# Performance work log

Measured on AMD Instinct MI355X. Metric: run time of the kernel, lower is better.

The kernel has to match this reference:

```python
import math
import jax, jax.numpy as jnp
import numpy as np

N = 10000      # num_nodes
E = 320000     # num_edges (avg degree 32)
D = 256        # hidden_dim
H = 8          # num_heads
HD = D // H    # head_dim = 32
S = 3          # num_scales
SCALES = (1.0, 2.0, 4.0)
BASE_MD = 500.0   # max_distance
RADIUS = 50.0     # spatial density radius


def setup_inputs() -> dict:
    key = jax.random.key(0)
    ks = jax.random.split(key, 24)
    nrm = lambda k, shape, s=0.02: jax.random.normal(k, shape, jnp.float32) * s
    return {
        "x": jax.random.normal(ks[0], (N, D), jnp.float32),
        "coords": jax.random.uniform(ks[1], (N, 2), jnp.float32) * 1000.0,
        "edge_index": jax.random.randint(ks[2], (2, E), 0, N, jnp.int32),
        "Wq": nrm(ks[3], (S, D, D)),
        "Wk": nrm(ks[4], (S, D, D)),
        "Wv": nrm(ks[5], (S, D, D)),
        "Wo": nrm(ks[6], (S, D, D)),
        "bo": jnp.zeros((S, D), jnp.float32),
        "temp": jnp.ones((S, H), jnp.float32),
        "dist_emb": nrm(ks[7], (S, 100, HD // 2)),
        "dir_emb": nrm(ks[8], (S, 16, HD // 2)),
        "Wsp1": nrm(ks[9], (S, HD, HD)),
        "bsp1": jnp.zeros((S, HD), jnp.float32),
        "Wsp2": nrm(ks[10], (S, 1, HD)),
        "bsp2": jnp.zeros((S, 1), jnp.float32),
        "Wd1": nrm(ks[11], (S, D // 2, 3)),
        "bd1": jnp.zeros((S, D // 2), jnp.float32),
        "Wd2": nrm(ks[12], (S, D, D // 2)),
        "bd2": jnp.zeros((S, D), jnp.float32),
        "Wf": nrm(ks[13], (D, S * D)),
        "bf": jnp.zeros((D,), jnp.float32),
    }


def reference(x, coords, edge_index, Wq, Wk, Wv, Wo, bo, temp, dist_emb, dir_emb,
              Wsp1, bsp1, Wsp2, bsp2, Wd1, bd1, Wd2, bd2, Wf, bf):
    src, dst = edge_index[0], edge_index[1]   # row=source j, col/dst=target i
    n = x.shape[0]
    eps = 1e-8

    # ---- shared density statistics (same math in every scale's encoder) ----
    ones_e = jnp.ones(src.shape[0], jnp.float32)
    deg = jax.ops.segment_sum(ones_e, src, num_segments=n)
    deg_n = deg / (deg.max() + eps)
    # spatial density: count of neighbors within RADIUS via full cdist (as in torch)
    c = jax.lax.stop_gradient(coords)  # only used via thresholds / integer bins -> zero grad
    d2 = jnp.sqrt(jnp.maximum(((c[:, None, :] - c[None, :, :]) ** 2).sum(-1), 0.0))
    sp = (d2 <= RADIUS).sum(axis=1).astype(jnp.float32) - 1.0
    sp = sp / (sp.max() + eps)
    # local feature variance
    nbr_sum = jax.ops.segment_sum(x[dst], src, num_segments=n)
    cnt = jnp.maximum(deg, 1.0)[:, None]
    fvar = jnp.linalg.norm(x - nbr_sum / cnt, axis=-1)
    fvar = fvar / (fvar.max() + eps)
    dens_raw = jnp.stack([deg_n, sp, fvar], axis=-1)  # [N, 3]

    # ---- shared relative geometry (binned -> no grad through coords) ----
    rel = c[src] - c[dst]                       # coords_j - coords_i
    dist = jnp.linalg.norm(rel, axis=-1)        # [E]
    ang = jnp.arctan2(rel[:, 1], rel[:, 0])
    abin = jnp.clip(((ang + math.pi) / (2.0 * math.pi) * 15.0).astype(jnp.int32), 0, 15)

    outs = []
    for s in range(S):
        md = BASE_MD * SCALES[s]
        dbin = jnp.clip((dist / md * 99.0).astype(jnp.int32), 0, 99)
        se = jnp.concatenate([dist_emb[s][dbin], dir_emb[s][abin]], axis=-1)  # [E, HD]
        enc = (jax.nn.relu(se @ Wsp1[s].T + bsp1[s]) @ Wsp2[s].T + bsp2[s])[:, 0]  # [E]

        df = jax.nn.relu(dens_raw @ Wd1[s].T + bd1[s]) @ Wd2[s].T + bd2[s]  # [N, D]

        q = (x @ Wq[s].T).reshape(n, H, HD)
        k = (x @ Wk[s].T).reshape(n, H, HD)
        v = (x @ Wv[s].T).reshape(n, H, HD)

        scores = (q[dst] * k[src]).sum(-1) / math.sqrt(HD)  # [E, H]
        scores = scores / temp[s][None, :]
        scores = scores + enc[:, None]
        dfi, dfj = df[dst], df[src]
        dsim = (dfi * dfj).sum(-1) / (jnp.maximum(jnp.linalg.norm(dfi, axis=-1), eps)
                                       * jnp.maximum(jnp.linalg.norm(dfj, axis=-1), eps))
        scores = scores * (1.0 + 0.5 * dsim[:, None])

        # scatter-softmax over edges grouped by destination node
        smax = jax.ops.segment_max(scores, dst, num_segments=n)
        p = jnp.exp(scores - smax[dst])
        z = jax.ops.segment_sum(p, dst, num_segments=n)
        probs = p / (z[dst] + 1e-16)

        agg = jax.ops.segment_sum(probs[..., None] * v[src], dst, num_segments=n)
        outs.append(agg.reshape(n, D) @ Wo[s].T + bo[s])

    fused = jnp.concatenate(outs, axis=-1) @ Wf.T + bf
    return fused
```

## Files before the change

kernel.cpp:

```cpp
#include <hip/hip_runtime.h>

typedef _Float16 f16;
typedef _Float16 f16x4 __attribute__((ext_vector_type(4)));
typedef _Float16 f16x8 __attribute__((ext_vector_type(8)));
typedef float    f32x4 __attribute__((ext_vector_type(4)));
typedef float    fv2   __attribute__((ext_vector_type(2)));

__device__ __forceinline__ float4 ld4h(const f16* p) {
  f16x4 t = *(const f16x4*)p;
  return make_float4((float)t[0], (float)t[1], (float)t[2], (float)t[3]);
}

__device__ __forceinline__ float4 dec_fp8x4(unsigned u) {
  fv2 lo = __builtin_amdgcn_cvt_pk_f32_fp8(u, false);
  fv2 hi = __builtin_amdgcn_cvt_pk_f32_fp8(u, true);
  return make_float4(lo[0], lo[1], hi[0], hi[1]);
}

__device__ __forceinline__ unsigned enc_fp8x4(float a, float b, float c, float d) {
  unsigned v = 0;
  v = __builtin_amdgcn_cvt_pk_fp8_f32(a, b, v, false);
  v = __builtin_amdgcn_cvt_pk_fp8_f32(c, d, v, true);
  return v;
}

__device__ __forceinline__ void gld_lds16(const void* g, void* l) {
  __builtin_amdgcn_global_load_lds(
      (const __attribute__((address_space(1))) unsigned*)g,
      (__attribute__((address_space(3))) unsigned*)l, 16, 0, 0);
}

__device__ __forceinline__ int cell_of(const float* coords, int i) {
  int cx = (int)(coords[2 * i] * 0.02f);
  int cy = (int)(coords[2 * i + 1] * 0.02f);
  cx = cx < 0 ? 0 : (cx > 19 ? 19 : cx);
  cy = cy < 0 ? 0 : (cy > 19 ? 19 : cy);
  return cy * 20 + cx;
}

__global__ __launch_bounds__(256) void prep_kernel(
    const float* __restrict__ x, const float* __restrict__ Wq, const float* __restrict__ Wk,
    const float* __restrict__ Wv, const float* __restrict__ Wd2,
    f16* __restrict__ x_h, unsigned* __restrict__ x8, f16* __restrict__ wqvk,
    f16* __restrict__ wd2h,
    const float* __restrict__ dist_emb, const float* __restrict__ dir_emb,
    const float* __restrict__ Wsp1, const float* __restrict__ bsp1,
    const float* __restrict__ Wsp2, const float* __restrict__ bsp2,
    float* __restrict__ enc_tab,
    const int* __restrict__ eidx, const float* __restrict__ coords,
    int* deg_i, int* indeg_i, int* cellcnt, int E, int N)
{
  const int b = blockIdx.x;
  if (b < 2048) {
    const int n0 = N * 64;
    const int total = n0 + 147456 + 24576;
    for (int i = b * 256 + threadIdx.x; i < total; i += 2048 * 256) {
      int k = i;
      if (k < n0) {
        float4 v = ((const float4*)x)[k];
        f16x4 o; o[0] = (f16)v.x; o[1] = (f16)v.y; o[2] = (f16)v.z; o[3] = (f16)v.w;
        ((f16x4*)x_h)[k] = o;
        x8[k] = enc_fp8x4(v.x, v.y, v.z, v.w);
        continue;
      }
      const float4* sp; f16x4* dp;
      k -= n0;
      if (k < 147456) {
        int s = k / 49152, r = k % 49152, m = r / 16384, off = r % 16384;
        const float* w = (m == 0) ? Wq : (m == 1) ? Wk : Wv;
        int dblk = (m == 0) ? 0 : (m == 1) ? 32768 : 16384;
        sp = (const float4*)(w + s * 65536) + off;
        dp = (f16x4*)wqvk + s * 49152 + dblk + off;
      } else {
        k -= 147456;
        sp = (const float4*)Wd2 + k; dp = (f16x4*)wd2h + k;
      }
      float4 v = *sp;
      f16x4 o; o[0] = (f16)v.x; o[1] = (f16)v.y; o[2] = (f16)v.z; o[3] = (f16)v.w;
      *dp = o;
    }
  } else if (b < 2067) {
    int id = (b - 2048) * 256 + threadIdx.x;
    if (id >= 3 * 1600) return;
    int s = id / 1600, c = id % 1600, db = c >> 4, ab = c & 15;
    const float* de = dist_emb + (size_t)(s * 100 + db) * 16;
    const float* ae = dir_emb + (size_t)(s * 16 + ab) * 16;
    const float* w1 = Wsp1 + s * 1024;
    const float* b1 = bsp1 + s * 32;
    const float* w2 = Wsp2 + s * 32;
    float enc = bsp2[s];
    for (int j = 0; j < 32; ++j) {
      float a = b1[j];
      const float* wr = w1 + j * 32;
#pragma unroll
      for (int i = 0; i < 16; ++i) a += de[i] * wr[i];
#pragma unroll
      for (int i = 0; i < 16; ++i) a += ae[i] * wr[16 + i];
      enc += fmaxf(a, 0.0f) * w2[j];
    }
    enc_tab[id] = enc;
  } else {
    int e = (b - 2067) * 256 + threadIdx.x;
    if (e < E) {
      atomicAdd(&deg_i[eidx[e]], 1);
      atomicAdd(&indeg_i[eidx[E + e]], 1);
    }
    if (e < N) atomicAdd(&cellcnt[cell_of(coords, e)], 1);
  }
}

__global__ __launch_bounds__(256) void wfo_kernel(
    const float* __restrict__ Wf, const float* __restrict__ Wo,
    const float* __restrict__ bo, const float* __restrict__ bf,
    f16* __restrict__ wfo, float* __restrict__ bias_f)
{
  const int j = threadIdx.x;
  if (blockIdx.y == 3) {
    if (blockIdx.x != 0) return;
    float acc = bf[j];
    const float* wr = Wf + (size_t)j * 768;
    for (int t = 0; t < 768; ++t) acc = fmaf(bo[t], wr[t], acc);
    bias_f[j] = acc;
    return;
  }
  __shared__ float wrow[256];
  const int o = blockIdx.x, s = blockIdx.y;
  wrow[j] = Wf[o * 768 + s * 256 + j];
  __syncthreads();
  const float* wo = Wo + (size_t)s * 65536 + j;
  float acc = 0.f;
#pragma unroll 8
  for (int m = 0; m < 256; ++m) acc = fmaf(wrow[m], wo[(size_t)m * 256], acc);
  wfo[(size_t)o * 768 + s * 256 + j] = (f16)acc;
}

__global__ __launch_bounds__(1024) void scan_kernel(const int* __restrict__ indeg,
                                                    const int* __restrict__ deg,
                                                    const int* __restrict__ cellcnt,
                                                    int* dptr, int* sptr, int* cptr,
                                                    int* __restrict__ perm, int N)
{
  __shared__ int lds[1024];
  __shared__ int cnt[256], scn2[256], fill[256];
  const int tid = threadIdx.x;
  const int pass = blockIdx.x;
  if (pass == 3) {
    if (tid < 256) { cnt[tid] = 0; fill[tid] = 0; }
    __syncthreads();
    for (int n = tid; n < N; n += 1024) {
      int d = indeg[n];
      int key = 255 - (d > 255 ? 255 : d);
      atomicAdd(&cnt[key], 1);
    }
    __syncthreads();
    if (tid < 256) scn2[tid] = cnt[tid];
    __syncthreads();
    for (int off = 1; off < 256; off <<= 1) {
      int v = 0;
      if (tid < 256 && tid >= off) v = scn2[tid - off];
      __syncthreads();
      if (tid < 256) scn2[tid] += v;
      __syncthreads();
    }
    for (int n = tid; n < N; n += 1024) {
      int d = indeg[n];
      int key = 255 - (d > 255 ? 255 : d);
      int pos = scn2[key] - cnt[key] + atomicAdd(&fill[key], 1);
      perm[pos] = n;
    }
    return;
  }
  const int* in = (pass == 0) ? indeg : (pass == 1) ? deg : cellcnt;
  int* out = (pass == 0) ? dptr : (pass == 1) ? sptr : cptr;
  int len = (pass == 2) ? 400 : N;
  int base = tid * 16;
  int loc[16];
  int sum = 0;
#pragma unroll
  for (int j = 0; j < 16; ++j) {
    int v = (base + j < len) ? in[base + j] : 0;
    loc[j] = sum; sum += v;
  }
  lds[tid] = sum;
  __syncthreads();
  for (int off = 1; off < 1024; off <<= 1) {
    int t = (tid >= off) ? lds[tid - off] : 0;
    __syncthreads();
    lds[tid] += t;
    __syncthreads();
  }
  int prev = tid ? lds[tid - 1] : 0;
#pragma unroll
  for (int j = 0; j < 16; ++j)
    if (base + j < len) out[base + j] = prev + loc[j];
  if (tid == 1023) out[len] = lds[1023];
}

__global__ __launch_bounds__(256) void scatter_kernel(
    const int* __restrict__ eidx, const float* __restrict__ coords,
    const int* __restrict__ dptr, const int* __restrict__ sptr, const int* __restrict__ cptr,
    int* fill_d, int* fill_s, int* fill_c,
    int2* __restrict__ erec, int* __restrict__ sdst, float2* __restrict__ scoord, int E, int N)
{
  int e = blockIdx.x * 256 + threadIdx.x;
  if (e < E) {
    int s = eidx[e], d = eidx[E + e];
    float rx = coords[2 * s] - coords[2 * d];
    float ry = coords[2 * s + 1] - coords[2 * d + 1];
    float dist = sqrtf(rx * rx + ry * ry);
    float ang = atan2f(ry, rx);
    int ab = (int)((ang + 3.14159265358979323846f) / 6.28318530717958647692f * 15.0f);
    ab = ab < 0 ? 0 : (ab > 15 ? 15 : ab);
    int b0 = (int)((dist / 500.0f) * 99.0f);  b0 = b0 < 0 ? 0 : (b0 > 99 ? 99 : b0);
    int b1 = (int)((dist / 1000.0f) * 99.0f); b1 = b1 < 0 ? 0 : (b1 > 99 ? 99 : b1);
    int b2 = (int)((dist / 2000.0f) * 99.0f); b2 = b2 < 0 ? 0 : (b2 > 99 ? 99 : b2);
    unsigned pb = (unsigned)b0 | ((unsigned)b1 << 7) | ((unsigned)b2 << 14) | ((unsigned)ab << 21);
    int pd = dptr[d] + atomicAdd(&fill_d[d], 1);
    erec[pd] = make_int2(s, (int)pb);
    int ps = sptr[s] + atomicAdd(&fill_s[s], 1);
    sdst[ps] = d;
  }
  if (e < N) {
    int cid = cell_of(coords, e);
    int pc = cptr[cid] + atomicAdd(&fill_c[cid], 1);
    scoord[pc] = ((const float2*)coords)[e];
  }
}

__global__ __launch_bounds__(256) void node_stats_kernel(
    const float* __restrict__ coords, const float2* __restrict__ scoord,
    const int* __restrict__ cptr,
    const float* __restrict__ x, const unsigned* __restrict__ x8,
    const int* __restrict__ sptr, const int* __restrict__ sdst,
    int* __restrict__ sp_i, float* __restrict__ fvar, int N)
{
  int wv = threadIdx.x >> 6, lane = threadIdx.x & 63;
  int node = blockIdx.x * 4 + wv;
  if (node >= N) return;

  float cx = coords[2 * node], cy = coords[2 * node + 1];
  {
    int gx = (int)(cx * 0.02f); gx = gx < 0 ? 0 : (gx > 19 ? 19 : gx);
    int gy = (int)(cy * 0.02f); gy = gy < 0 ? 0 : (gy > 19 ? 19 : gy);
    int x0 = gx > 0 ? gx - 1 : 0, x1 = gx < 19 ? gx + 1 : 19;
    int y0 = gy > 0 ? gy - 1 : 0, y1 = gy < 19 ? gy + 1 : 19;
    int cnt = 0;
    for (int r = y0; r <= y1; ++r) {
      int j0 = cptr[r * 20 + x0], j1 = cptr[r * 20 + x1 + 1];
      for (int j = j0 + lane; j < j1; j += 64) {
        float2 c = scoord[j];
        float dx = cx - c.x, dy = cy - c.y;
        cnt += (dx * dx + dy * dy <= 2500.0f) ? 1 : 0;
      }
    }
    cnt += __shfl_xor(cnt, 1);  cnt += __shfl_xor(cnt, 2);  cnt += __shfl_xor(cnt, 4);
    cnt += __shfl_xor(cnt, 8);  cnt += __shfl_xor(cnt, 16); cnt += __shfl_xor(cnt, 32);
    if (lane == 0) sp_i[node] = cnt;
  }

  const int slot = lane >> 3, w = lane & 7;
  float sum[32];
#pragma unroll
  for (int i = 0; i < 32; ++i) sum[i] = 0.f;
  int e0 = sptr[node], e1 = sptr[node + 1];
  int nit = (e1 - e0 + 7) >> 3;
  for (int it = 0; it < nit; ++it) {
    int e = e0 + it * 8 + slot;
    bool valid = e < e1;
    int dd = sdst[valid ? e : e1 - 1];
    const unsigned* xp = x8 + dd * 64 + w * 8;
    uint4 a = *(const uint4*)xp;
    uint4 b = *(const uint4*)(xp + 4);
    float vm = valid ? 1.f : 0.f;
    unsigned wd[8] = {a.x, a.y, a.z, a.w, b.x, b.y, b.z, b.w};
#pragma unroll
    for (int k = 0; k < 8; ++k) {
      float4 f = dec_fp8x4(wd[k]);
      sum[k*4+0] = fmaf(vm, f.x, sum[k*4+0]);
      sum[k*4+1] = fmaf(vm, f.y, sum[k*4+1]);
      sum[k*4+2] = fmaf(vm, f.z, sum[k*4+2]);
      sum[k*4+3] = fmaf(vm, f.w, sum[k*4+3]);
    }
  }
#pragma unroll
  for (int i = 0; i < 32; ++i) {
    sum[i] += __shfl_xor(sum[i], 8);
    sum[i] += __shfl_xor(sum[i], 16);
    sum[i] += __shfl_xor(sum[i], 32);
  }
  float rcnt = 1.0f / fmaxf((float)(e1 - e0), 1.0f);
  const float4* xp4 = (const float4*)(x + (size_t)node * 256 + w * 32);
  float ss = 0.f;
#pragma unroll
  for (int k = 0; k < 8; ++k) {
    float4 xm = xp4[k];
    float d0 = xm.x - sum[k*4+0] * rcnt;
    float d1 = xm.y - sum[k*4+1] * rcnt;
    float d2 = xm.z - sum[k*4+2] * rcnt;
    float d3 = xm.w - sum[k*4+3] * rcnt;
    ss += d0*d0 + d1*d1 + d2*d2 + d3*d3;
  }
  ss += __shfl_xor(ss, 1);  ss += __shfl_xor(ss, 2);  ss += __shfl_xor(ss, 4);
  ss += __shfl_xor(ss, 8);  ss += __shfl_xor(ss, 16); ss += __shfl_xor(ss, 32);
  if (lane == 0) fvar[node] = sqrtf(ss * 0.125f);
}

__global__ __launch_bounds__(1024) void maxred_kernel(
    const int* __restrict__ sptr, const int* __restrict__ sp_i,
    const float* __restrict__ fvar, float* __restrict__ maxf, int N)
{
  __shared__ float l0[1024], l1[1024], l2[1024];
  int tid = threadIdx.x;
  float m0 = 0.f, m1 = 0.f, m2 = 0.f;
  for (int i = tid; i < N; i += 1024) {
    m0 = fmaxf(m0, (float)(sptr[i + 1] - sptr[i]));
    m1 = fmaxf(m1, (float)(sp_i[i] - 1));
    m2 = fmaxf(m2, fvar[i]);
  }
  l0[tid] = m0; l1[tid] = m1; l2[tid] = m2;
  __syncthreads();
  for (int off = 512; off > 0; off >>= 1) {
    if (tid < off) {
      l0[tid] = fmaxf(l0[tid], l0[tid + off]);
      l1[tid] = fmaxf(l1[tid], l1[tid + off]);
      l2[tid] = fmaxf(l2[tid], l2[tid + off]);
    }
    __syncthreads();
  }
  if (tid == 0) { maxf[0] = l0[0]; maxf[1] = l1[0]; maxf[2] = l2[0]; }
}

__global__ __launch_bounds__(256) void h_kernel(
    const int* __restrict__ sptr, const int* __restrict__ sp_i, const float* __restrict__ fvar,
    const float* __restrict__ maxf, const float* __restrict__ Wd1,
    const float* __restrict__ bd1, f16* __restrict__ hbuf, int N, int Mp)
{
  int id = blockIdx.x * 256 + threadIdx.x;
  if (id >= N * 128) return;
  int s = blockIdx.y;
  int node = id >> 7, j = id & 127;
  float dm = maxf[0] + 1e-8f;
  float sm = maxf[1] + 1e-8f;
  float fm = maxf[2] + 1e-8f;
  float d0 = (float)(sptr[node + 1] - sptr[node]) / dm;
  float d1 = (float)(sp_i[node] - 1) / sm;
  float d2 = fvar[node] / fm;
  const float* wr = Wd1 + s * 384 + j * 3;
  float h = fmaxf(wr[0] * d0 + wr[1] * d1 + wr[2] * d2 + bd1[s * 128 + j], 0.0f);
  hbuf[(size_t)s * Mp * 128 + (size_t)node * 128 + j] = (f16)h;
}

__global__ __launch_bounds__(256) void gemm_bt_f16(
    const f16* __restrict__ A, int lda, long sA,
    const f16* __restrict__ B, int ldb, long sB,
    const float* __restrict__ bias, int sBias,
    void* __restrict__ Cv, int ldc, long sC, int K, int Mstore, int outMode,
    unsigned char* __restrict__ Cv2, int ldc2, long sC2, int ysplit)
{
  __shared__ f16 As[128 * 64];
  __shared__ f16 Bs[128 * 64];
  const int s = blockIdx.z;
  const int tid = threadIdx.x;
  const int lane = tid & 63;
  const int w = tid >> 6;
  const int wr = (w >> 1) * 64, wc = (w & 1) * 64;
  const int srow = tid >> 3;
  const int scol = (((tid & 7) ^ (srow & 7))) * 8;
  const f16* Ab = A + (size_t)s * sA + (size_t)(blockIdx.x * 128 + srow) * lda + scol;
  const f16* Bb = B + (size_t)s * sB + (size_t)(blockIdx.y * 128 + srow) * ldb + scol;
  char* Asl = (char*)As + tid * 16;
  char* Bsl = (char*)Bs + tid * 16;

  f32x4 acc[4][4] = {};

  for (int kt = 0; kt < K; kt += 64) {
    __syncthreads();
#pragma unroll
    for (int i = 0; i < 4; ++i) {
      gld_lds16(Ab + (size_t)i * 32 * lda + kt, Asl + i * 4096);
      gld_lds16(Bb + (size_t)i * 32 * ldb + kt, Bsl + i * 4096);
    }
    __syncthreads();
#pragma unroll
    for (int kq = 0; kq < 2; ++kq) {
      const int krd = kq * 32 + (lane >> 4) * 8;
      const int kc = krd >> 3;
      f16x8 af[4], bfr[4];
#pragma unroll
      for (int t = 0; t < 4; ++t) {
        const int ra = wr + t * 16 + (lane & 15);
        const int rb = wc + t * 16 + (lane & 15);
        af[t]  = *(const f16x8*)&As[ra * 64 + (kc ^ (ra & 7)) * 8];
        bfr[t] = *(const f16x8*)&Bs[rb * 64 + (kc ^ (rb & 7)) * 8];
      }
#pragma unroll
      for (int mi = 0; mi < 4; ++mi)
#pragma unroll
        for (int ni = 0; ni < 4; ++ni)
          acc[mi][ni] = __builtin_amdgcn_mfma_f32_16x16x32_f16(af[mi], bfr[ni], acc[mi][ni], 0, 0, 0);
    }
  }

  const int r0 = (lane >> 4) << 2;
  const int c0 = lane & 15;
  const bool f8p = ((int)blockIdx.y >= ysplit);
  const int cbase = f8p ? ((int)blockIdx.y - ysplit) * 128 : (int)blockIdx.y * 128;
#pragma unroll
  for (int mi = 0; mi < 4; ++mi) {
#pragma unroll
    for (int ni = 0; ni < 4; ++ni) {
      int col = cbase + wc + ni * 16 + c0;
      float bv = (!f8p && bias) ? bias[s * sBias + col] : 0.0f;
#pragma unroll
      for (int r = 0; r < 4; ++r) {
        int row = blockIdx.x * 128 + wr + mi * 16 + r0 + r;
        if (row < Mstore) {
          float v = acc[mi][ni][r] + bv;
          if (f8p) {
            unsigned pk = __builtin_amdgcn_cvt_pk_fp8_f32(v, v, 0u, false);
            Cv2[(size_t)s * sC2 + (size_t)row * ldc2 + col] = (unsigned char)(pk & 0xffu);
          } else if (outMode == 1) {
            ((f16*)Cv)[(size_t)s * sC + (size_t)row * ldc + col] = (f16)v;
          } else {
            ((float*)Cv)[(size_t)s * sC + (size_t)row * ldc + col] = v;
          }
        }
      }
    }
  }
}

__global__ __launch_bounds__(256) void norm_kernel(const f16* __restrict__ dfh,
                                                   unsigned* __restrict__ drec8, int N, int Mp)
{
  int wv = threadIdx.x >> 6, lane = threadIdx.x & 63;
  int node = blockIdx.x * 4 + wv;
  if (node >= N) return;
  int s = blockIdx.y;
  float4 d = ld4h(dfh + (size_t)s * Mp * 256 + (size_t)node * 256 + lane * 4);
  float ss = d.x * d.x + d.y * d.y + d.z * d.z + d.w * d.w;
  ss += __shfl_xor(ss, 1);  ss += __shfl_xor(ss, 2);  ss += __shfl_xor(ss, 4);
  ss += __shfl_xor(ss, 8);  ss += __shfl_xor(ss, 16); ss += __shfl_xor(ss, 32);
  float rn = 1.0f / fmaxf(sqrtf(ss), 1e-8f);
  drec8[(size_t)s * Mp * 64 + node * 64 + lane] = enc_fp8x4(d.x * rn, d.y * rn, d.z * rn, d.w * rn);
}

__global__ __launch_bounds__(256) void edge_attn(
    const f16* __restrict__ nrec0, const unsigned* __restrict__ krec0,
    const unsigned* __restrict__ drec0, const int2* __restrict__ erec,
    const int* __restrict__ dptr, const int* __restrict__ perm,
    const float* __restrict__ enc_tab, const float* __restrict__ temp,
    f16* __restrict__ aggc, int N, int Mp)
{
  int wv = threadIdx.x >> 6, lane = threadIdx.x & 63;
  int node = blockIdx.x * 4 + wv;
  if (node >= N) return;
  node = perm[node];
  const int s = blockIdx.y;
  const int sshift = 7 * s;
  const f16* nrec = nrec0 + (size_t)s * Mp * 512;
  const unsigned* krec8 = krec0 + (size_t)s * Mp * 64;
  const unsigned* drec8 = drec0 + (size_t)s * Mp * 64;
  const float* enc_s = enc_tab + s * 1600;

  const int slot = lane >> 4;
  const int sub  = lane & 15;
  const int hd   = sub >> 1;
  const int half = sub & 1;
  const int doff = hd * 8 + half * 4;
  const int voff = hd * 32 + half * 16;

  float qf[16];
  {
    const f16* qp = nrec + (size_t)node * 512 + voff;
    f16x8 a = *(const f16x8*)qp;
    f16x8 b = *(const f16x8*)(qp + 8);
#pragma unroll
    for (int j = 0; j < 8; ++j) { qf[j] = (float)a[j]; qf[8 + j] = (float)b[j]; }
  }
  uint4 diw = *(const uint4*)(drec8 + node * 64 + doff);
  const float inv_th = 0.17677669529663687f / temp[s * 8 + hd];

  float m = -1e30f, z = 0.f;
  float acc[16];
#pragma unroll
  for (int i = 0; i < 16; ++i) acc[i] = 0.f;

  int e0 = dptr[node], e1 = dptr[node + 1];
  int nit = (e1 - e0 + 3) >> 2;
  for (int it = 0; it < nit; ++it) {
    int e = e0 + it * 4 + slot;
    bool valid = e < e1;
    int2 rec = erec[valid ? e : e1 - 1];
    int src = rec.x;
    unsigned pb = (unsigned)rec.y;
    uint4 kwv = *(const uint4*)(krec8 + src * 64 + doff);
    uint4 dwv = *(const uint4*)(drec8 + src * 64 + doff);
    const f16* vp = nrec + (size_t)src * 512 + 256 + voff;
    f16x8 vs0 = *(const f16x8*)vp;
    f16x8 vs1 = *(const f16x8*)(vp + 8);
    float enc = enc_s[((pb >> sshift) & 127u) * 16 + (pb >> 21)];

    unsigned kw[4] = {kwv.x, kwv.y, kwv.z, kwv.w};
    unsigned dw[4] = {dwv.x, dwv.y, dwv.z, dwv.w};
    unsigned di[4] = {diw.x, diw.y, diw.z, diw.w};
    float qk0 = 0.f, qk1 = 0.f, ds0 = 0.f, ds1 = 0.f;
#pragma unroll
    for (int w = 0; w < 4; ++w) {
      float4 kf = dec_fp8x4(kw[w]);
      qk0 = fmaf(qf[w*4+0], kf.x, qk0);
      qk1 = fmaf(qf[w*4+1], kf.y, qk1);
      qk0 = fmaf(qf[w*4+2], kf.z, qk0);
      qk1 = fmaf(qf[w*4+3], kf.w, qk1);
      float4 df = dec_fp8x4(dw[w]);
      float4 dd = dec_fp8x4(di[w]);
      ds0 = fmaf(dd.x, df.x, ds0);
      ds1 = fmaf(dd.y, df.y, ds1);
      ds0 = fmaf(dd.z, df.z, ds0);
      ds1 = fmaf(dd.w, df.w, ds1);
    }
    float qk = qk0 + qk1;
    float ds = ds0 + ds1;
    qk += __shfl_xor(qk, 1);
    ds += __shfl_xor(ds, 1); ds += __shfl_xor(ds, 2);
    ds += __shfl_xor(ds, 4); ds += __shfl_xor(ds, 8);

    float sc = (qk * inv_th + enc) * (1.0f + 0.5f * ds);
    sc = valid ? sc : -1e30f;
    if (__any(sc > m + 8.0f)) {
      float mn = fmaxf(m, sc);
      float rs = __expf(m - mn);
      z *= rs;
#pragma unroll
      for (int i = 0; i < 16; ++i) acc[i] *= rs;
      m = mn;
    }
    float p = __expf(sc - m) * (valid ? 1.0f : 0.0f);
    z += p;
#pragma unroll
    for (int j = 0; j < 8; ++j) acc[j]     = fmaf(p, (float)vs0[j], acc[j]);
#pragma unroll
    for (int j = 0; j < 8; ++j) acc[8 + j] = fmaf(p, (float)vs1[j], acc[8 + j]);
  }

  float M = m;
  M = fmaxf(M, __shfl_xor(M, 16));
  M = fmaxf(M, __shfl_xor(M, 32));
  float f = __expf(m - M);
  z *= f;
  z += __shfl_xor(z, 16); z += __shfl_xor(z, 32);
#pragma unroll
  for (int i = 0; i < 16; ++i) {
    float a = acc[i] * f;
    a += __shfl_xor(a, 16); a += __shfl_xor(a, 32);
    acc[i] = a;
  }
  float rz = 1.0f / (z + 1e-16f);
  if (slot == 0) {
    f16* op = aggc + (size_t)node * 768 + s * 256 + voff;
    f16x8 o0, o1;
#pragma unroll
    for (int j = 0; j < 8; ++j) { o0[j] = (f16)(acc[j] * rz); o1[j] = (f16)(acc[8 + j] * rz); }
    *(f16x8*)op = o0;
    *(f16x8*)(op + 8) = o1;
  }
}

extern "C" void kernel_launch(void* const* d_in, const int* in_sizes, int n_in,
                              void* d_out, int out_size, void* d_ws, size_t ws_size,
                              hipStream_t stream)
{
  const float* x      = (const float*)d_in[0];
  const float* coords = (const float*)d_in[1];
  const int*   eidx   = (const int*)  d_in[2];
  const float* Wq   = (const float*)d_in[3];
  const float* Wk   = (const float*)d_in[4];
  const float* Wv   = (const float*)d_in[5];
  const float* Wo   = (const float*)d_in[6];
  const float* bo   = (const float*)d_in[7];
  const float* temp = (const float*)d_in[8];
  const float* dist_emb = (const float*)d_in[9];
  const float* dir_emb  = (const float*)d_in[10];
  const float* Wsp1 = (const float*)d_in[11];
  const float* bsp1 = (const float*)d_in[12];
  const float* Wsp2 = (const float*)d_in[13];
  const float* bsp2 = (const float*)d_in[14];
  const float* Wd1  = (const float*)d_in[15];
  const float* bd1  = (const float*)d_in[16];
  const float* Wd2  = (const float*)d_in[17];
  const float* bd2  = (const float*)d_in[18];
  const float* Wf   = (const float*)d_in[19];
  const float* bf   = (const float*)d_in[20];
  (void)n_in; (void)out_size; (void)ws_size;

  const int N  = in_sizes[0] / 256;
  const int E  = in_sizes[2] / 2;
  const int Mp = ((N + 127) / 128) * 128;

  char* p = (char*)d_ws;
  auto alloc = [&](size_t b) -> void* {
    void* r = (void*)p;
    p += (b + 255) & ~(size_t)255;
    return r;
  };

  f16*      x_h   = (f16*)     alloc((size_t)Mp * 256 * 2);
  unsigned* x8    = (unsigned*)alloc((size_t)Mp * 256);
  f16*      nrec3 = (f16*)     alloc((size_t)3 * Mp * 512 * 2);
  unsigned* krec3 = (unsigned*)alloc((size_t)3 * Mp * 256);
  unsigned* drec3 = (unsigned*)alloc((size_t)3 * Mp * 256);
  f16*      hbuf3 = (f16*)     alloc((size_t)3 * Mp * 128 * 2);
  f16*      dfh3  = (f16*)     alloc((size_t)3 * Mp * 256 * 2);
  f16*      aggc  = (f16*)     alloc((size_t)Mp * 768 * 2);
  f16*      wqvk  = (f16*)     alloc((size_t)3 * 768 * 256 * 2);
  f16*      wfo   = (f16*)     alloc((size_t)256 * 768 * 2);
  float*    bias_f = (float*)  alloc(256 * 4);
  f16*      wd2h  = (f16*)     alloc((size_t)3 * 256 * 128 * 2);
  float*    enc_tab = (float*) alloc((size_t)3 * 1600 * 4);
  int*    dptr = (int*)   alloc((size_t)(N + 1) * 4);
  int*    sptr = (int*)   alloc((size_t)(N + 1) * 4);
  int*    cptr = (int*)   alloc((size_t)401 * 4);
  int*    perm = (int*)   alloc((size_t)N * 4);
  int2*   erec = (int2*)  alloc((size_t)E * 8);
  int*    sdst = (int*)   alloc((size_t)E * 4);
  float2* scoord = (float2*)alloc((size_t)N * 8);
  float*  fvar = (float*) alloc((size_t)N * 4);
  int*    sp_i = (int*)   alloc((size_t)N * 4);
  float*  maxf = (float*) alloc(4 * 4);
  char* z0 = p;
  int* deg_i   = (int*)alloc((size_t)N * 4);
  int* indeg_i = (int*)alloc((size_t)N * 4);
  int* fill_d  = (int*)alloc((size_t)N * 4);
  int* fill_s  = (int*)alloc((size_t)N * 4);
  int* cellcnt = (int*)alloc(400 * 4);
  int* fill_c  = (int*)alloc(400 * 4);
  size_t zbytes = (size_t)(p - z0);
  hipMemsetAsync(z0, 0, zbytes, stream);

  {
    int histBlocks = (E + 255) / 256;
    prep_kernel<<<2067 + histBlocks, 256, 0, stream>>>(
        x, Wq, Wk, Wv, Wd2, x_h, x8, wqvk, wd2h,
        dist_emb, dir_emb, Wsp1, bsp1, Wsp2, bsp2, enc_tab,
        eidx, coords, deg_i, indeg_i, cellcnt, E, N);
  }
  wfo_kernel<<<dim3(256, 4), 256, 0, stream>>>(Wf, Wo, bo, bf, wfo, bias_f);
  scan_kernel<<<4, 1024, 0, stream>>>(indeg_i, deg_i, cellcnt, dptr, sptr, cptr, perm, N);
  scatter_kernel<<<(E + 255) / 256, 256, 0, stream>>>(eidx, coords, dptr, sptr, cptr,
                                                      fill_d, fill_s, fill_c, erec, sdst, scoord, E, N);
  node_stats_kernel<<<(N + 3) / 4, 256, 0, stream>>>(coords, scoord, cptr, x, x8,
                                                     sptr, sdst, sp_i, fvar, N);
  maxred_kernel<<<1, 1024, 0, stream>>>(sptr, sp_i, fvar, maxf, N);

  const int mtiles = Mp / 128;
  h_kernel<<<dim3((N * 128 + 255) / 256, 3), 256, 0, stream>>>(sptr, sp_i, fvar, maxf,
                                                               Wd1, bd1, hbuf3, N, Mp);
  gemm_bt_f16<<<dim3(mtiles, 2, 3), 256, 0, stream>>>(hbuf3, 128, (long)Mp * 128,
                                                      wd2h, 128, 32768, bd2, 256,
                                                      dfh3, 256, (long)Mp * 256, 128, Mp, 1,
                                                      nullptr, 0, 0, 99);
  norm_kernel<<<dim3((N + 3) / 4, 3), 256, 0, stream>>>(dfh3, drec3, N, Mp);
  gemm_bt_f16<<<dim3(mtiles, 6, 3), 256, 0, stream>>>(x_h, 256, 0,
                                                      wqvk, 256, 196608, nullptr, 0,
                                                      nrec3, 512, (long)Mp * 512, 256, Mp, 1,
                                                      (unsigned char*)krec3, 256, (long)Mp * 256, 4);
  edge_attn<<<dim3((N + 3) / 4, 3), 256, 0, stream>>>(nrec3, krec3, drec3, erec, dptr, perm,
                                                      enc_tab, temp, aggc, N, Mp);
  gemm_bt_f16<<<dim3(mtiles, 2, 1), 256, 0, stream>>>(aggc, 768, 0,
                                                      wfo, 768, 0, bias_f, 0,
                                                      d_out, 256, 0, 768, N, 0,
                                                      nullptr, 0, 0, 99);
}
```

Before: 386.3 us.

## Fuse density MLP layer into Wd2 GEMM, merge wfo into prep, prefetch edge records

Computes the first density MLP layer (relu of Wd1 times the density features) directly into the GEMM's LDS A tile, which removes the h_kernel launch and the hbuf round trip through global memory. The Wf·Wo folding blocks are merged into prep_kernel as extra blocks, saving one launch. In edge_attn the next edge record is software-prefetched one iteration ahead to hide gather latency. The costs are some redundant per-tile recomputation of h and slightly higher register pressure in the attention loop.

```diff
diff --git a/kernel.cpp b/kernel.cpp
--- a/kernel.cpp
+++ b/kernel.cpp
@@ -48,7 +48,11 @@
     const float* __restrict__ Wsp2, const float* __restrict__ bsp2,
     float* __restrict__ enc_tab,
     const int* __restrict__ eidx, const float* __restrict__ coords,
-    int* deg_i, int* indeg_i, int* cellcnt, int E, int N)
+    int* deg_i, int* indeg_i, int* cellcnt,
+    const float* __restrict__ Wf, const float* __restrict__ Wo,
+    const float* __restrict__ bo, const float* __restrict__ bf,
+    f16* __restrict__ wfo, float* __restrict__ bias_f,
+    int E, int N, int hb)
 {
   const int b = blockIdx.x;
   if (b < 2048) {
@@ -99,39 +103,32 @@
       enc += fmaxf(a, 0.0f) * w2[j];
     }
     enc_tab[id] = enc;
-  } else {
+  } else if (b < 2067 + hb) {
     int e = (b - 2067) * 256 + threadIdx.x;
     if (e < E) {
       atomicAdd(&deg_i[eidx[e]], 1);
       atomicAdd(&indeg_i[eidx[E + e]], 1);
     }
     if (e < N) atomicAdd(&cellcnt[cell_of(coords, e)], 1);
-  }
-}
-
-__global__ __launch_bounds__(256) void wfo_kernel(
-    const float* __restrict__ Wf, const float* __restrict__ Wo,
-    const float* __restrict__ bo, const float* __restrict__ bf,
-    f16* __restrict__ wfo, float* __restrict__ bias_f)
-{
-  const int j = threadIdx.x;
-  if (blockIdx.y == 3) {
-    if (blockIdx.x != 0) return;
+  } else if (b < 2067 + hb + 768) {
+    __shared__ float wrow[256];
+    int idx = b - (2067 + hb);
+    int s = idx >> 8, o = idx & 255;
+    int j = threadIdx.x;
+    wrow[j] = Wf[o * 768 + s * 256 + j];
+    __syncthreads();
+    const float* wo = Wo + (size_t)s * 65536 + j;
+    float acc = 0.f;
+#pragma unroll 8
+    for (int m = 0; m < 256; ++m) acc = fmaf(wrow[m], wo[(size_t)m * 256], acc);
+    wfo[(size_t)o * 768 + s * 256 + j] = (f16)acc;
+  } else {
+    int j = threadIdx.x;
     float acc = bf[j];
     const float* wr = Wf + (size_t)j * 768;
     for (int t = 0; t < 768; ++t) acc = fmaf(bo[t], wr[t], acc);
     bias_f[j] = acc;
-    return;
-  }
-  __shared__ float wrow[256];
-  const int o = blockIdx.x, s = blockIdx.y;
-  wrow[j] = Wf[o * 768 + s * 256 + j];
-  __syncthreads();
-  const float* wo = Wo + (size_t)s * 65536 + j;
-  float acc = 0.f;
-#pragma unroll 8
-  for (int m = 0; m < 256; ++m) acc = fmaf(wrow[m], wo[(size_t)m * 256], acc);
-  wfo[(size_t)o * 768 + s * 256 + j] = (f16)acc;
+  }
 }
 
 __global__ __launch_bounds__(1024) void scan_kernel(const int* __restrict__ indeg,
@@ -330,24 +327,90 @@
   if (tid == 0) { maxf[0] = l0[0]; maxf[1] = l1[0]; maxf[2] = l2[0]; }
 }
 
-__global__ __launch_bounds__(256) void h_kernel(
+__global__ __launch_bounds__(256) void gemm_wd2(
     const int* __restrict__ sptr, const int* __restrict__ sp_i, const float* __restrict__ fvar,
-    const float* __restrict__ maxf, const float* __restrict__ Wd1,
-    const float* __restrict__ bd1, f16* __restrict__ hbuf, int N, int Mp)
-{
-  int id = blockIdx.x * 256 + threadIdx.x;
-  if (id >= N * 128) return;
-  int s = blockIdx.y;
-  int node = id >> 7, j = id & 127;
-  float dm = maxf[0] + 1e-8f;
-  float sm = maxf[1] + 1e-8f;
-  float fm = maxf[2] + 1e-8f;
-  float d0 = (float)(sptr[node + 1] - sptr[node]) / dm;
-  float d1 = (float)(sp_i[node] - 1) / sm;
-  float d2 = fvar[node] / fm;
-  const float* wr = Wd1 + s * 384 + j * 3;
-  float h = fmaxf(wr[0] * d0 + wr[1] * d1 + wr[2] * d2 + bd1[s * 128 + j], 0.0f);
-  hbuf[(size_t)s * Mp * 128 + (size_t)node * 128 + j] = (f16)h;
+    const float* __restrict__ maxf, const float* __restrict__ Wd1, const float* __restrict__ bd1,
+    const f16* __restrict__ B, const float* __restrict__ bd2,
+    f16* __restrict__ dfh, int N, int Mp)
+{
+  __shared__ f16 As[128 * 64];
+  __shared__ f16 Bs[128 * 64];
+  const int s = blockIdx.z;
+  const int tid = threadIdx.x;
+  const int lane = tid & 63;
+  const int w = tid >> 6;
+  const int wr = (w >> 1) * 64, wc = (w & 1) * 64;
+  const int srow = tid >> 3;
+  const int c = tid & 7;
+  const int scolB = ((c ^ (srow & 7))) * 8;
+  const f16* Bb = B + (size_t)s * 32768 + (size_t)(blockIdx.y * 128 + srow) * 128 + scolB;
+  char* Bsl = (char*)Bs + tid * 16;
+  const float dm = maxf[0] + 1e-8f, sm = maxf[1] + 1e-8f, fm = maxf[2] + 1e-8f;
+
+  f32x4 acc[4][4] = {};
+
+  for (int kt = 0; kt < 128; kt += 64) {
+    __syncthreads();
+#pragma unroll
+    for (int i = 0; i < 4; ++i)
+      gld_lds16(Bb + (size_t)i * 32 * 128 + kt, Bsl + i * 4096);
+#pragma unroll
+    for (int i = 0; i < 4; ++i) {
+      int r = srow + i * 32;
+      int node = blockIdx.x * 128 + r;
+      float d0 = 0.f, d1 = 0.f, d2 = 0.f;
+      if (node < N) {
+        d0 = (float)(sptr[node + 1] - sptr[node]) / dm;
+        d1 = (float)(sp_i[node] - 1) / sm;
+        d2 = fvar[node] / fm;
+      }
+      int kc8 = c ^ (r & 7);
+      const float* w1 = Wd1 + s * 384 + (kt + kc8 * 8) * 3;
+      const float* b1 = bd1 + s * 128 + kt + kc8 * 8;
+      f16x8 hv;
+#pragma unroll
+      for (int j = 0; j < 8; ++j) {
+        float h = fmaf(w1[j*3], d0, fmaf(w1[j*3+1], d1, fmaf(w1[j*3+2], d2, b1[j])));
+        hv[j] = (f16)fmaxf(h, 0.f);
+      }
+      *(f16x8*)&As[r * 64 + c * 8] = hv;
+    }
+    __syncthreads();
+#pragma unroll
+    for (int kq = 0; kq < 2; ++kq) {
+      const int krd = kq * 32 + (lane >> 4) * 8;
+      const int kc = krd >> 3;
+      f16x8 af[4], bfr[4];
+#pragma unroll
+      for (int t = 0; t < 4; ++t) {
+        const int ra = wr + t * 16 + (lane & 15);
+        const int rb = wc + t * 16 + (lane & 15);
+        af[t]  = *(const f16x8*)&As[ra * 64 + (kc ^ (ra & 7)) * 8];
+        bfr[t] = *(const f16x8*)&Bs[rb * 64 + (kc ^ (rb & 7)) * 8];
+      }
+#pragma unroll
+      for (int mi = 0; mi < 4; ++mi)
+#pragma unroll
+        for (int ni = 0; ni < 4; ++ni)
+          acc[mi][ni] = __builtin_amdgcn_mfma_f32_16x16x32_f16(af[mi], bfr[ni], acc[mi][ni], 0, 0, 0);
+    }
+  }
+
+  const int r0 = (lane >> 4) << 2;
+  const int c0 = lane & 15;
+#pragma unroll
+  for (int mi = 0; mi < 4; ++mi) {
+#pragma unroll
+    for (int ni = 0; ni < 4; ++ni) {
+      int col = blockIdx.y * 128 + wc + ni * 16 + c0;
+      float bv = bd2[s * 256 + col];
+#pragma unroll
+      for (int r = 0; r < 4; ++r) {
+        int row = blockIdx.x * 128 + wr + mi * 16 + r0 + r;
+        dfh[(size_t)s * Mp * 256 + (size_t)row * 256 + col] = (f16)(acc[mi][ni][r] + bv);
+      }
+    }
+  }
 }
 
 __global__ __launch_bounds__(256) void gemm_bt_f16(
@@ -488,59 +551,67 @@
 
   int e0 = dptr[node], e1 = dptr[node + 1];
   int nit = (e1 - e0 + 3) >> 2;
-  for (int it = 0; it < nit; ++it) {
-    int e = e0 + it * 4 + slot;
-    bool valid = e < e1;
-    int2 rec = erec[valid ? e : e1 - 1];
-    int src = rec.x;
-    unsigned pb = (unsigned)rec.y;
-    uint4 kwv = *(const uint4*)(krec8 + src * 64 + doff);
-    uint4 dwv = *(const uint4*)(drec8 + src * 64 + doff);
-    const f16* vp = nrec + (size_t)src * 512 + 256 + voff;
-    f16x8 vs0 = *(const f16x8*)vp;
-    f16x8 vs1 = *(const f16x8*)(vp + 8);
-    float enc = enc_s[((pb >> sshift) & 127u) * 16 + (pb >> 21)];
-
-    unsigned kw[4] = {kwv.x, kwv.y, kwv.z, kwv.w};
-    unsigned dw[4] = {dwv.x, dwv.y, dwv.z, dwv.w};
-    unsigned di[4] = {diw.x, diw.y, diw.z, diw.w};
-    float qk0 = 0.f, qk1 = 0.f, ds0 = 0.f, ds1 = 0.f;
-#pragma unroll
-    for (int w = 0; w < 4; ++w) {
-      float4 kf = dec_fp8x4(kw[w]);
-      qk0 = fmaf(qf[w*4+0], kf.x, qk0);
-      qk1 = fmaf(qf[w*4+1], kf.y, qk1);
-      qk0 = fmaf(qf[w*4+2], kf.z, qk0);
-      qk1 = fmaf(qf[w*4+3], kf.w, qk1);
-      float4 df = dec_fp8x4(dw[w]);
-      float4 dd = dec_fp8x4(di[w]);
-      ds0 = fmaf(dd.x, df.x, ds0);
-      ds1 = fmaf(dd.y, df.y, ds1);
-      ds0 = fmaf(dd.z, df.z, ds0);
-      ds1 = fmaf(dd.w, df.w, ds1);
-    }
-    float qk = qk0 + qk1;
-    float ds = ds0 + ds1;
-    qk += __shfl_xor(qk, 1);
-    ds += __shfl_xor(ds, 1); ds += __shfl_xor(ds, 2);
-    ds += __shfl_xor(ds, 4); ds += __shfl_xor(ds, 8);
-
-    float sc = (qk * inv_th + enc) * (1.0f + 0.5f * ds);
-    sc = valid ? sc : -1e30f;
-    if (__any(sc > m + 8.0f)) {
-      float mn = fmaxf(m, sc);
-      float rs = __expf(m - mn);
-      z *= rs;
-#pragma unroll
-      for (int i = 0; i < 16; ++i) acc[i] *= rs;
-      m = mn;
-    }
-    float p = __expf(sc - m) * (valid ? 1.0f : 0.0f);
-    z += p;
-#pragma unroll
-    for (int j = 0; j < 8; ++j) acc[j]     = fmaf(p, (float)vs0[j], acc[j]);
-#pragma unroll
-    for (int j = 0; j < 8; ++j) acc[8 + j] = fmaf(p, (float)vs1[j], acc[8 + j]);
+  if (nit > 0) {
+    int ce = e0 + slot; if (ce >= e1) ce = e1 - 1;
+    int2 recA = erec[ce];
+    for (int it = 0; it < nit; ++it) {
+      int en = e0 + (it + 1) * 4 + slot; en = (en < e1) ? en : e1 - 1;
+      int2 recN = erec[en];
+
+      int e = e0 + it * 4 + slot;
+      bool valid = e < e1;
+      int src = recA.x;
+      unsigned pb = (unsigned)recA.y;
+      uint4 kwv = *(const uint4*)(krec8 + src * 64 + doff);
+      uint4 dwv = *(const uint4*)(drec8 + src * 64 + doff);
+      const f16* vp = nrec + (size_t)src * 512 + 256 + voff;
+      f16x8 vs0 = *(const f16x8*)vp;
+      f16x8 vs1 = *(const f16x8*)(vp + 8);
+      float enc = enc_s[((pb >> sshift) & 127u) * 16 + (pb >> 21)];
+
+      unsigned kw[4] = {kwv.x, kwv.y, kwv.z, kwv.w};
+      unsigned dw[4] = {dwv.x, dwv.y, dwv.z, dwv.w};
+      unsigned di[4] = {diw.x, diw.y, diw.z, diw.w};
+      float qk0 = 0.f, qk1 = 0.f, ds0 = 0.f, ds1 = 0.f;
+#pragma unroll
+      for (int w = 0; w < 4; ++w) {
+        float4 kf = dec_fp8x4(kw[w]);
+        qk0 = fmaf(qf[w*4+0], kf.x, qk0);
+        qk1 = fmaf(qf[w*4+1], kf.y, qk1);
+        qk0 = fmaf(qf[w*4+2], kf.z, qk0);
+        qk1 = fmaf(qf[w*4+3], kf.w, qk1);
+        float4 df = dec_fp8x4(dw[w]);
+        float4 dd = dec_fp8x4(di[w]);
+        ds0 = fmaf(dd.x, df.x, ds0);
+        ds1 = fmaf(dd.y, df.y, ds1);
+        ds0 = fmaf(dd.z, df.z, ds0);
+        ds1 = fmaf(dd.w, df.w, ds1);
+      }
+      float qk = qk0 + qk1;
+      float ds = ds0 + ds1;
+      qk += __shfl_xor(qk, 1);
+      ds += __shfl_xor(ds, 1); ds += __shfl_xor(ds, 2);
+      ds += __shfl_xor(ds, 4); ds += __shfl_xor(ds, 8);
+
+      float sc = (qk * inv_th + enc) * (1.0f + 0.5f * ds);
+      sc = valid ? sc : -1e30f;
+      if (__any(sc > m + 8.0f)) {
+        float mn = fmaxf(m, sc);
+        float rs = __expf(m - mn);
+        z *= rs;
+#pragma unroll
+        for (int i = 0; i < 16; ++i) acc[i] *= rs;
+        m = mn;
+      }
+      float p = __expf(sc - m) * (valid ? 1.0f : 0.0f);
+      z += p;
+#pragma unroll
+      for (int j = 0; j < 8; ++j) acc[j]     = fmaf(p, (float)vs0[j], acc[j]);
+#pragma unroll
+      for (int j = 0; j < 8; ++j) acc[8 + j] = fmaf(p, (float)vs1[j], acc[8 + j]);
+
+      recA = recN;
+    }
   }
 
   float M = m;
@@ -609,7 +680,6 @@
   f16*      nrec3 = (f16*)     alloc((size_t)3 * Mp * 512 * 2);
   unsigned* krec3 = (unsigned*)alloc((size_t)3 * Mp * 256);
   unsigned* drec3 = (unsigned*)alloc((size_t)3 * Mp * 256);
-  f16*      hbuf3 = (f16*)     alloc((size_t)3 * Mp * 128 * 2);
   f16*      dfh3  = (f16*)     alloc((size_t)3 * Mp * 256 * 2);
   f16*      aggc  = (f16*)     alloc((size_t)Mp * 768 * 2);
   f16*      wqvk  = (f16*)     alloc((size_t)3 * 768 * 256 * 2);
@@ -637,14 +707,12 @@
   size_t zbytes = (size_t)(p - z0);
   hipMemsetAsync(z0, 0, zbytes, stream);
 
-  {
-    int histBlocks = (E + 255) / 256;
-    prep_kernel<<<2067 + histBlocks, 256, 0, stream>>>(
-        x, Wq, Wk, Wv, Wd2, x_h, x8, wqvk, wd2h,
-        dist_emb, dir_emb, Wsp1, bsp1, Wsp2, bsp2, enc_tab,
-        eidx, coords, deg_i, indeg_i, cellcnt, E, N);
-  }
-  wfo_kernel<<<dim3(256, 4), 256, 0, stream>>>(Wf, Wo, bo, bf, wfo, bias_f);
+  const int hb = (E + 255) / 256;
+  prep_kernel<<<2067 + hb + 768 + 1, 256, 0, stream>>>(
+      x, Wq, Wk, Wv, Wd2, x_h, x8, wqvk, wd2h,
+      dist_emb, dir_emb, Wsp1, bsp1, Wsp2, bsp2, enc_tab,
+      eidx, coords, deg_i, indeg_i, cellcnt,
+      Wf, Wo, bo, bf, wfo, bias_f, E, N, hb);
   scan_kernel<<<4, 1024, 0, stream>>>(indeg_i, deg_i, cellcnt, dptr, sptr, cptr, perm, N);
   scatter_kernel<<<(E + 255) / 256, 256, 0, stream>>>(eidx, coords, dptr, sptr, cptr,
                                                       fill_d, fill_s, fill_c, erec, sdst, scoord, E, N);
@@ -653,12 +721,8 @@
   maxred_kernel<<<1, 1024, 0, stream>>>(sptr, sp_i, fvar, maxf, N);
 
   const int mtiles = Mp / 128;
-  h_kernel<<<dim3((N * 128 + 255) / 256, 3), 256, 0, stream>>>(sptr, sp_i, fvar, maxf,
-                                                               Wd1, bd1, hbuf3, N, Mp);
-  gemm_bt_f16<<<dim3(mtiles, 2, 3), 256, 0, stream>>>(hbuf3, 128, (long)Mp * 128,
-                                                      wd2h, 128, 32768, bd2, 256,
-                                                      dfh3, 256, (long)Mp * 256, 128, Mp, 1,
-                                                      nullptr, 0, 0, 99);
+  gemm_wd2<<<dim3(mtiles, 2, 3), 256, 0, stream>>>(sptr, sp_i, fvar, maxf, Wd1, bd1,
+                                                   wd2h, bd2, dfh3, N, Mp);
   norm_kernel<<<dim3((N + 3) / 4, 3), 256, 0, stream>>>(dfh3, drec3, N, Mp);
   gemm_bt_f16<<<dim3(mtiles, 6, 3), 256, 0, stream>>>(x_h, 256, 0,
                                                       wqvk, 256, 196608, nullptr, 0,
```

After: 336.3 us. 13.0% less time.
